# Kernel optimization log

Hardware: AMD Instinct MI355X
Metric: run time of the kernel (lower is better)

The kernel has to match this reference:

```python
import jax, jax.numpy as jnp
import numpy as np

B, T, N = 2048, 500, 64
DT = 0.25  # integration step
V_TH = 30.0

# Izhikevich behaviour params: (a, b, c, d, v0); u0 = b * v0
LLBN_P = (0.02, 0.20, -65.0, 6.0, -70.0)   # LLBN_behaviour (tonic-spiking-like)
EBN_P  = (0.02, 0.25, -55.0, 0.05, -64.0)  # phasic bursting
IFN_P  = (0.02, 0.25, -65.0, 6.0, -64.0)   # phasic spiking
TN_P   = (0.02, 0.20, -50.0, 2.0, -70.0)   # tonic bursting
MN_P   = IFN_P                              # phasic spiking


def izh_step(v, u, I, p):
    """One Euler step of the Izhikevich neuron; returns (spike, v_new, u_new)."""
    a, b, c, d, _ = p
    v_ = v + DT * (0.04 * v * v + 5.0 * v + 140.0 - u + I)
    u_ = u + DT * a * (b * v - u)
    z = (v_ >= V_TH).astype(v.dtype)
    v_new = jnp.where(z > 0, c, v_)
    u_new = u_ + z * d
    return z, v_new, u_new


def init_state(p, batch):
    a, b, c, d, v0 = p
    return jnp.full((batch,), v0, jnp.float32), jnp.full((batch,), b * v0, jnp.float32)


def setup_inputs() -> dict:
    key = jax.random.key(0)
    k1, k2 = jax.random.split(key)
    input_mat = jax.random.uniform(k1, (B, T, N), dtype=jnp.float32)
    weights_matrix = jax.random.uniform(k2, (24,), dtype=jnp.float32)
    return {"input_mat": input_mat, "weights_matrix": weights_matrix}


def _run(input_mat, w):
    # summed retinal drive per timestep; [B, T] -> [T, B] for scan
    zp1 = (input_mat * w[0]).sum(-1).T
    zp2 = (input_mat * w[12]).sum(-1).T

    vL, uL = init_state(LLBN_P, B); zL = jnp.zeros((B,), jnp.float32)
    vE, uE = init_state(EBN_P, B)
    vI, uI = init_state(IFN_P, B)
    vT, uT = init_state(TN_P, B); zT = jnp.zeros((B,), jnp.float32)
    vM, uM = init_state(MN_P, B)
    # channel 2 uses the SAME cells (self.LLBN/EBN/... are reused in the
    # original forward, so weights w[2],w[3],w[9],w[10] apply) with its own state
    vL2, uL2 = vL, uL; zL2 = zL
    vE2, uE2 = vE, uE
    vI2, uI2 = vI, uI
    vT2, uT2 = vT, uT; zT2 = zT
    vM2, uM2 = vM, uM

    carry0 = (vL, uL, zL, vE, uE, vI, uI, vT, uT, zT, vM, uM,
              vL2, uL2, zL2, vE2, uE2, vI2, uI2, vT2, uT2, zT2, vM2, uM2)

    def step(carry, zin):
        (vL, uL, zL, vE, uE, vI, uI, vT, uT, zT, vM, uM,
         vL2, uL2, zL2, vE2, uE2, vI2, uI2, vT2, uT2, zT2, vM2, uM2) = carry
        zp, zp2 = zin
        # --- channel 1 ---  (temp feedback is always 0 in the original: local var)
        z2, vL, uL = izh_step(vL, uL, w[2] * (zp * w[1]) + w[3] * zL, LLBN_P)
        z3, vE, uE = izh_step(vE, uE, zp * w[4] + z2 * w[5], EBN_P)
        z4, vI, uI = izh_step(vI, uI, z3 * w[6], IFN_P)
        z5, vT, uT = izh_step(vT, uT, w[9] * (z3 * w[8]) + w[10] * zT, TN_P)
        z6, vM, uM = izh_step(vM, uM, z5 * w[11], MN_P)
        # --- channel 2 ---
        z22, vL2, uL2 = izh_step(vL2, uL2, w[2] * (zp2 * w[13]) + w[3] * zL2, LLBN_P)
        z32, vE2, uE2 = izh_step(vE2, uE2, zp2 * w[16] + z22 * w[17], EBN_P)
        z42, vI2, uI2 = izh_step(vI2, uI2, z32 * w[18], IFN_P)
        z52, vT2, uT2 = izh_step(vT2, uT2, w[9] * (z32 * w[20]) + w[10] * zT2, TN_P)
        z62, vM2, uM2 = izh_step(vM2, uM2, z52 * w[23], MN_P)
        new_carry = (vL, uL, z2, vE, uE, vI, uI, vT, uT, z5, vM, uM,
                     vL2, uL2, z22, vE2, uE2, vI2, uI2, vT2, uT2, z52, vM2, uM2)
        outs = (z6, vM, z62, vM2,
                jnp.stack([z2, z3, z4, z5], -1),   # o_spikes_o [B,4]
                jnp.stack([vL, vE, vI, vT], -1))   # v_o        [B,4]
        return new_carry, outs

    _, (o_spikes, v, o_spikes2, v2, o_spikes_o, v_o) = jax.lax.scan(step, carry0, (zp1, zp2))
    # scan stacks on leading T axis -> move to [B, T, ...]
    tr = lambda a: jnp.moveaxis(a, 0, 1)
    return tr(o_spikes), tr(v), tr(o_spikes2), tr(v2), tr(o_spikes_o), tr(v_o)


def reference(input_mat, weights_matrix):
    return _run(input_mat, weights_matrix)
```

## Files before the change

### kernel.cpp

```cpp
#include <hip/hip_runtime.h>

#define B_ 2048
#define T_ 500
#define BT (B_ * T_)

__device__ __forceinline__ float izh_m(float& v, float& u, float I,
                                       float b, float c, float d, bool valid) {
    float t  = 0.04f * v * v + 5.0f * v + 140.0f - u + I;
    float v_ = v + 0.25f * t;
    float u_ = u + 0.005f * (b * v - u);
    float z  = (v_ >= 30.0f) ? 1.0f : 0.0f;
    float vn = (v_ >= 30.0f) ? c : v_;
    float un = u_ + z * d;
    if (!valid) { z = 0.f; vn = v; un = u; }
    v = vn; u = un;
    return z;
}

__global__ __launch_bounds__(192) void fused_scan_kernel(
        const float* __restrict__ in, const float* __restrict__ w24,
        float* __restrict__ out) {
    __shared__ float S_lds[128];
    __shared__ float ring[32 * 56];

    const int tid   = threadIdx.x;
    const int wid   = tid >> 6;
    const int lane  = tid & 63;
    const int bbase = blockIdx.x << 2;

    const int c    = lane >> 4;
    const int slot = lane & 15;
    const int chl  = slot >> 3;
    const int role = slot & 7;

    const float a0   = chl ? w24[12] : w24[0];
    const float W1v  = chl ? w24[13] : w24[1];
    const float W4v  = chl ? w24[16] : w24[4];
    const float W5v  = chl ? w24[17] : w24[5];
    const float W6v  = chl ? w24[18] : w24[6];
    const float W8v  = chl ? w24[20] : w24[8];
    const float W11v = chl ? w24[23] : w24[11];
    const float W2 = w24[2], W3 = w24[3], W9 = w24[9], W10 = w24[10];

    float pb, pcc, pd, v, u, wA, wB, wC, wD;
    float fL = 0.f, fE = 0.f, fITM = 0.f;
    int offs, srcRole;
    if (role == 0) {
        pb=0.20f; pcc=-65.f; pd=6.f;   v=-70.f; u=-14.f;
        wA=W2;  wB=W1v;  wC=0.f; wD=W3;  offs=0; srcRole=0; fL=1.f;
    } else if (role == 1) {
        pb=0.25f; pcc=-55.f; pd=0.05f; v=-64.f; u=-16.f;
        wA=1.f; wB=W4v;  wC=W5v; wD=0.f; offs=3; srcRole=0; fE=1.f;
    } else if (role == 2) {
        pb=0.25f; pcc=-65.f; pd=6.f;   v=-64.f; u=-16.f;
        wA=1.f; wB=W6v;  wC=0.f; wD=0.f; offs=6; srcRole=1; fITM=1.f;
    } else if (role == 3) {
        pb=0.20f; pcc=-50.f; pd=2.f;   v=-70.f; u=-14.f;
        wA=W9;  wB=W8v;  wC=0.f; wD=W10; offs=6; srcRole=1; fITM=1.f;
    } else if (role == 4) {
        pb=0.25f; pcc=-65.f; pd=6.f;   v=-64.f; u=-16.f;
        wA=1.f; wB=W11v; wC=0.f; wD=0.f; offs=9; srcRole=3; fITM=1.f;
    } else {
        pb=0.25f; pcc=-65.f; pd=6.f;   v=-64.f; u=-16.f;
        wA=0.f; wB=0.f;  wC=0.f; wD=0.f; offs=9; srcRole=0;
    }
    const bool wr = (chl == 0 && role <= 4) || (chl == 1 && role == 4);
    const int  p  = (chl == 0) ? role : 5;
    const int srcLane = (c << 4) | (chl << 3) | srcRole;
    const int ringoff = c * 14 + 2 * p;

    float z_last = 0.f, in_p1 = 0.f, in_p2 = 0.f;
    float zp1 = 0.f, zp2 = 0.f, zp3 = 0.f;

    const int lw = wid - 1;

#define REDUCE_WRITE(VV, ROW, I_) {                                            \
    float s_ = ((VV).x + (VV).y) + ((VV).z + (VV).w);                          \
    s_ += __shfl_xor(s_, 1);                                                   \
    s_ += __shfl_xor(s_, 2);                                                   \
    s_ += __shfl_xor(s_, 4);                                                   \
    s_ += __shfl_xor(s_, 8);                                                   \
    if ((lane & 15) == 0) sw[(ROW) * 16 + (I_) * 4 + (lane >> 4)] = s_;        \
}

#define LOAD_GROUP(KK) {                                                       \
    float* sw = S_lds + ((KK) & 1) * 64;                                       \
    const int t0l = 16 * (KK);                                                 \
    const int row0 = lw * 2;                                                   \
    const float4* gb0 = (const float4*)(in + ((size_t)(bbase + row0) * T_ + t0l) * 64);     \
    const float4* gb1 = (const float4*)(in + ((size_t)(bbase + row0 + 1) * T_ + t0l) * 64); \
    float4 v00, v01, v02, v03, v10, v11, v12, v13;                             \
    if (t0l + 15 < T_) {                                                       \
        v00 = gb0[lane]; v01 = gb0[64 + lane];                                 \
        v02 = gb0[128 + lane]; v03 = gb0[192 + lane];                          \
        v10 = gb1[lane]; v11 = gb1[64 + lane];                                 \
        v12 = gb1[128 + lane]; v13 = gb1[192 + lane];                          \
    } else {                          \
        float4 zz = make_float4(0.f, 0.f, 0.f, 0.f);                           \
        v00 = gb0[lane]; v01 = zz; v02 = zz; v03 = zz;                         \
        v10 = gb1[lane]; v11 = zz; v12 = zz; v13 = zz;                         \
    }                                                                          \
    REDUCE_WRITE(v00, row0, 0)     REDUCE_WRITE(v01, row0, 1)                  \
    REDUCE_WRITE(v02, row0, 2)     REDUCE_WRITE(v03, row0, 3)                  \
    REDUCE_WRITE(v10, row0 + 1, 0) REDUCE_WRITE(v11, row0 + 1, 1)              \
    REDUCE_WRITE(v12, row0 + 1, 2) REDUCE_WRITE(v13, row0 + 1, 3)              \
}

#define SYS_ITER(SV, VEXPR, I_) {                                              \
    float in0 = in_p2;                                                         \
    in_p2 = in_p1;                                                             \
    in_p1 = __shfl(z_last, srcLane, 64);                                       \
    float zpc = (SV) * a0;                                                     \
    float X = (fL * zpc + fE * zp3) + fITM * in0;                              \
    float Isyn = wA * (X * wB) + wC * in0 + wD * z_last;                       \
    float znew = izh_m(v, u, Isyn, pb, pcc, pd, (VEXPR));                      \
    if (wr) *(float2*)(ringp + (I_) * 56) = make_float2(znew, v);              \
    zp3 = zp2; zp2 = zp1; zp1 = zpc;                                           \
    z_last = znew;                                                             \
}

#define GROUP16(VF)                                                            \
    SYS_ITER(g0.x, VF(0),  0)  SYS_ITER(g0.y, VF(1),  1)                       \
    SYS_ITER(g0.z, VF(2),  2)  SYS_ITER(g0.w, VF(3),  3)                       \
    SYS_ITER(g1.x, VF(4),  4)  SYS_ITER(g1.y, VF(5),  5)                       \
    SYS_ITER(g1.z, VF(6),  6)  SYS_ITER(g1.w, VF(7),  7)                       \
    SYS_ITER(g2.x, VF(8),  8)  SYS_ITER(g2.y, VF(9),  9)                       \
    SYS_ITER(g2.z, VF(10), 10) SYS_ITER(g2.w, VF(11), 11)                      \
    SYS_ITER(g3.x, VF(12), 12) SYS_ITER(g3.y, VF(13), 13)                      \
    SYS_ITER(g3.z, VF(14), 14) SYS_ITER(g3.w, VF(15), 15)

#define VF_PRO(i)  ((i) >= offs)
#define VF_ONE(i)  true
#define VF_EPI(i)  ((i) <= 3 + offs)

#define DUMP(K) {                                                              \
    const int td = lane & 15;                                                  \
    const int cc = lane >> 4;                                                  \
    const int t  = 16 * (K) - 9 + td;                                          \
    if (0 <= t && t <= 499) {                                                  \
        const float* rb = ring + cc * 14;                                      \
        float2 a2 = *(const float2*)&rb[((t)     & 31) * 56 + 0];              \
        float2 b2 = *(const float2*)&rb[((t + 3) & 31) * 56 + 2];              \
        float2 c1 = *(const float2*)&rb[((t + 6) & 31) * 56 + 4];              \
        float2 c2 = *(const float2*)&rb[((t + 6) & 31) * 56 + 6];              \
        float2 e1 = *(const float2*)&rb[((t + 9) & 31) * 56 + 8];              \
        float2 e2 = *(const float2*)&rb[((t + 9) & 31) * 56 + 10];             \
        const size_t g = (size_t)(bbase + cc) * T_ + t;                        \
        out[g]          = e1.x;                           \
        out[BT + g]     = e1.y;                           \
        out[2 * BT + g] = e2.x;                           \
        out[3 * BT + g] = e2.y;                           \
        ((float4*)out)[BT + g]     = make_float4(a2.x, b2.x, c1.x, c2.x);      \
        ((float4*)out)[2 * BT + g] = make_float4(a2.y, b2.y, c1.y, c2.y);      \
    }                                                                          \
}

    if (wid) { LOAD_GROUP(0) }
    __syncthreads();

    for (int k = 0; k <= 30; ++k) {
        if (wid == 0) {
            const float4* sp = (const float4*)(S_lds + (k & 1) * 64 + c * 16);
            float4 g0 = sp[0], g1 = sp[1], g2 = sp[2], g3 = sp[3];
            float* ringp = ring + (k & 1) * 896 + ringoff;
            if (k == 0) { GROUP16(VF_PRO) } else { GROUP16(VF_ONE) }
            DUMP(k)
        } else {
            LOAD_GROUP(k + 1)
        }
        __syncthreads();
    }
    if (wid == 0) {
        const float4* sp = (const float4*)(S_lds + 64 + c * 16);
        float4 g0 = sp[0], g1 = sp[1], g2 = sp[2], g3 = sp[3];
        float* ringp = ring + 896 + ringoff;
        GROUP16(VF_EPI)
        DUMP(31)
    }

#undef REDUCE_WRITE
#undef LOAD_GROUP
#undef SYS_ITER
#undef GROUP16
#undef VF_PRO
#undef VF_ONE
#undef VF_EPI
#undef DUMP
}

extern "C" void kernel_launch(void* const* d_in, const int* in_sizes, int n_in,
                              void* d_out, int out_size, void* d_ws, size_t ws_size,
                              hipStream_t stream) {
    const float* in = (const float*)d_in[0];
    const float* w  = (const float*)d_in[1];
    float* out = (float*)d_out;

    fused_scan_kernel<<<512, 192, 0, stream>>>(in, w, out);
}
```

Baseline: 79.30 us.

## Use single loader wave with register double-buffered prefetch of input groups

Replaces the two loader waves with one, so the block now has one scan wave and one loader wave (128 threads). The loader double-buffers in registers: it issues global loads for group k+2 into one register set while reducing group k+1 from the other, and the loop is unrolled by two to alternate buffers. The aim is to hide global load latency behind the scan wave's compute while using fewer threads per block. The risk is that one wave now carries all the load bandwidth and more registers, which could make the loader the bottleneck.

```diff
diff --git a/kernel.cpp b/kernel.cpp
--- a/kernel.cpp
+++ b/kernel.cpp
@@ -17,7 +17,7 @@
     return z;
 }
 
-__global__ __launch_bounds__(192) void fused_scan_kernel(
+__global__ __launch_bounds__(128) void fused_scan2_kernel(
         const float* __restrict__ in, const float* __restrict__ w24,
         float* __restrict__ out) {
     __shared__ float S_lds[128];
@@ -72,38 +72,37 @@
     float z_last = 0.f, in_p1 = 0.f, in_p2 = 0.f;
     float zp1 = 0.f, zp2 = 0.f, zp3 = 0.f;
 
-    const int lw = wid - 1;
-
-#define REDUCE_WRITE(VV, ROW, I_) {                                            \
-    float s_ = ((VV).x + (VV).y) + ((VV).z + (VV).w);                          \
-    s_ += __shfl_xor(s_, 1);                                                   \
-    s_ += __shfl_xor(s_, 2);                                                   \
-    s_ += __shfl_xor(s_, 4);                                                   \
-    s_ += __shfl_xor(s_, 8);                                                   \
-    if ((lane & 15) == 0) sw[(ROW) * 16 + (I_) * 4 + (lane >> 4)] = s_;        \
-}
-
-#define LOAD_GROUP(KK) {                                                       \
+    const float* inb = in + (size_t)bbase * T_ * 64;
+    float4 Ae[8], Ao[8], Be[8], Bo[8];
+
+#define ISSUE(KK, BE, BO) {                                                    \
+    const int t0i = 16 * (KK);                                                 \
+    _Pragma("unroll")                                                          \
+    for (int pp = 0; pp < 8; ++pp) {                                           \
+        const int rt = pp * 8 + (lane >> 3);                                   \
+        const int row = rt >> 4, tt = rt & 15;                                 \
+        const int tcl = (t0i + tt <= 499) ? tt : 0;                            \
+        const float* ap = inb + ((size_t)row * T_ + t0i + tcl) * 64            \
+                              + (lane & 7) * 8;                                \
+        BE[pp] = *(const float4*)ap;                                           \
+        BO[pp] = *(const float4*)(ap + 4);                                     \
+    }                                                                          \
+}
+
+#define REDUCE(KK, BE, BO) {                                                   \
     float* sw = S_lds + ((KK) & 1) * 64;                                       \
-    const int t0l = 16 * (KK);                                                 \
-    const int row0 = lw * 2;                                                   \
-    const float4* gb0 = (const float4*)(in + ((size_t)(bbase + row0) * T_ + t0l) * 64);     \
-    const float4* gb1 = (const float4*)(in + ((size_t)(bbase + row0 + 1) * T_ + t0l) * 64); \
-    float4 v00, v01, v02, v03, v10, v11, v12, v13;                             \
-    if (t0l + 15 < T_) {                                                       \
-        v00 = gb0[lane]; v01 = gb0[64 + lane];                                 \
-        v02 = gb0[128 + lane]; v03 = gb0[192 + lane];                          \
-        v10 = gb1[lane]; v11 = gb1[64 + lane];                                 \
-        v12 = gb1[128 + lane]; v13 = gb1[192 + lane];                          \
-    } else {                          \
-        float4 zz = make_float4(0.f, 0.f, 0.f, 0.f);                           \
-        v00 = gb0[lane]; v01 = zz; v02 = zz; v03 = zz;                         \
-        v10 = gb1[lane]; v11 = zz; v12 = zz; v13 = zz;                         \
+    const int t0r = 16 * (KK);                                                 \
+    _Pragma("unroll")                                                          \
+    for (int pp = 0; pp < 8; ++pp) {                                           \
+        float4 e = BE[pp], o = BO[pp];                                         \
+        float s = ((e.x + e.y) + (e.z + e.w)) + ((o.x + o.y) + (o.z + o.w));   \
+        s += __shfl_xor(s, 1);                                                 \
+        s += __shfl_xor(s, 2);                                                 \
+        s += __shfl_xor(s, 4);                                                 \
+        const int rt = pp * 8 + (lane >> 3);                                   \
+        const int row = rt >> 4, tt = rt & 15;                                 \
+        if ((lane & 7) == 0) sw[row * 16 + tt] = (t0r + tt <= 499) ? s : 0.f;  \
     }                                                                          \
-    REDUCE_WRITE(v00, row0, 0)     REDUCE_WRITE(v01, row0, 1)                  \
-    REDUCE_WRITE(v02, row0, 2)     REDUCE_WRITE(v03, row0, 3)                  \
-    REDUCE_WRITE(v10, row0 + 1, 0) REDUCE_WRITE(v11, row0 + 1, 1)              \
-    REDUCE_WRITE(v12, row0 + 1, 2) REDUCE_WRITE(v13, row0 + 1, 3)              \
 }
 
 #define SYS_ITER(SV, VEXPR, I_) {                                              \
@@ -155,37 +154,47 @@
     }                                                                          \
 }
 
-    if (wid) { LOAD_GROUP(0) }
+#define SCANP(K, VFSEL) {                                                      \
+    const float4* sp = (const float4*)(S_lds + ((K) & 1) * 64 + c * 16);       \
+    float4 g0 = sp[0], g1 = sp[1], g2 = sp[2], g3 = sp[3];                     \
+    float* ringp = ring + ((K) & 1) * 896 + ringoff;                           \
+    GROUP16(VFSEL)                                                             \
+    DUMP(K)                                                                    \
+}
+
+    if (wid == 1) {
+        ISSUE(0, Ae, Ao)
+        REDUCE(0, Ae, Ao)
+        ISSUE(1, Be, Bo)
+    }
     __syncthreads();
 
-    for (int k = 0; k <= 30; ++k) {
+    for (int k = 0; k < 32; k += 2) {
         if (wid == 0) {
-            const float4* sp = (const float4*)(S_lds + (k & 1) * 64 + c * 16);
-            float4 g0 = sp[0], g1 = sp[1], g2 = sp[2], g3 = sp[3];
-            float* ringp = ring + (k & 1) * 896 + ringoff;
-            if (k == 0) { GROUP16(VF_PRO) } else { GROUP16(VF_ONE) }
-            DUMP(k)
+            if (k == 0) { SCANP(k, VF_PRO) } else { SCANP(k, VF_ONE) }
         } else {
-            LOAD_GROUP(k + 1)
+            if (k + 2 < 32) { ISSUE(k + 2, Ae, Ao) }
+            if (k + 1 < 32) { REDUCE(k + 1, Be, Bo) }
+        }
+        __syncthreads();
+        if (wid == 0) {
+            if (k + 1 == 31) { SCANP(k + 1, VF_EPI) } else { SCANP(k + 1, VF_ONE) }
+        } else {
+            if (k + 3 < 32) { ISSUE(k + 3, Be, Bo) }
+            if (k + 2 < 32) { REDUCE(k + 2, Ae, Ao) }
         }
         __syncthreads();
     }
-    if (wid == 0) {
-        const float4* sp = (const float4*)(S_lds + 64 + c * 16);
-        float4 g0 = sp[0], g1 = sp[1], g2 = sp[2], g3 = sp[3];
-        float* ringp = ring + 896 + ringoff;
-        GROUP16(VF_EPI)
-        DUMP(31)
-    }
-
-#undef REDUCE_WRITE
-#undef LOAD_GROUP
+
+#undef ISSUE
+#undef REDUCE
 #undef SYS_ITER
 #undef GROUP16
 #undef VF_PRO
 #undef VF_ONE
 #undef VF_EPI
 #undef DUMP
+#undef SCANP
 }
 
 extern "C" void kernel_launch(void* const* d_in, const int* in_sizes, int n_in,
@@ -195,5 +204,5 @@
     const float* w  = (const float*)d_in[1];
     float* out = (float*)d_out;
 
-    fused_scan_kernel<<<512, 192, 0, stream>>>(in, w, out);
-}
+    fused_scan2_kernel<<<512, 128, 0, stream>>>(in, w, out);
+}
```

New measurement: 73.47 us. 7.4% less time.
